# Kernel tuning notes

Measured on AMD Instinct MI355X. Metric: run time of the kernel, lower is better.

## Reference

```python
import jax, jax.numpy as jnp
import numpy as np

D_MODEL = 1024
D_HEAD = 128
BATCH = 4
SEQ = 4096


def setup_inputs() -> dict:
    key = jax.random.key(0)
    ks = jax.random.split(key, 7)
    s = 1.0 / np.sqrt(D_MODEL)
    return {
        "x": jax.random.normal(ks[0], (BATCH, SEQ, D_MODEL), dtype=jnp.float32),
        "Wq": jax.random.normal(ks[1], (D_MODEL, D_HEAD), dtype=jnp.float32) * s,
        "bq": jax.random.normal(ks[2], (D_HEAD,), dtype=jnp.float32) * 0.02,
        "Wk": jax.random.normal(ks[3], (D_MODEL, D_HEAD), dtype=jnp.float32) * s,
        "bk": jax.random.normal(ks[4], (D_HEAD,), dtype=jnp.float32) * 0.02,
        "Wv": jax.random.normal(ks[5], (D_MODEL, D_HEAD), dtype=jnp.float32) * s,
        "bv": jax.random.normal(ks[6], (D_HEAD,), dtype=jnp.float32) * 0.02,
    }


def reference(x, Wq, bq, Wk, bk, Wv, bv):
    # Single-head causal self-attention (intended math of MaskedAttention).
    # x: [B, S, D_MODEL]; projections to [B, S, D_HEAD].
    q = x @ Wq + bq
    k = x @ Wk + bk
    v = x @ Wv + bv
    scale = 1.0 / jnp.sqrt(jnp.asarray(D_HEAD, dtype=x.dtype))
    scores = jnp.einsum("bsd,btd->bst", q, k) * scale  # [B, S, S]
    # additive causal mask: -inf strictly above the diagonal
    s_len = scores.shape[-1]
    causal = jnp.tril(jnp.ones((s_len, s_len), dtype=bool))
    scores = jnp.where(causal[None, :, :], scores, jnp.asarray(-jnp.inf, dtype=scores.dtype))
    attn = jax.nn.softmax(scores, axis=-1)
    return jnp.einsum("bst,btd->bsd", attn, v)  # [B, S, D_HEAD]
```

## Files before the change

kernel.cpp:

```cpp
#include <hip/hip_runtime.h>
#include <stdint.h>
#include <stddef.h>

#define SEQ 4096
#define DM 1024
#define DH 128
#define NB 4
#define SPLITS 4

typedef __attribute__((ext_vector_type(8))) short bf16x8;
typedef __attribute__((ext_vector_type(4))) float f32x4;

__device__ __forceinline__ unsigned short f2bf(float f) {
    union { float f; uint32_t u; } v; v.f = f;
    uint32_t u = v.u + 0x7FFF + ((v.u >> 16) & 1);
    return (unsigned short)(u >> 16);
}

__device__ __forceinline__ void gload_lds16(const void* g, void* l) {
    __builtin_amdgcn_global_load_lds(
        (const __attribute__((address_space(1))) void*)g,
        (__attribute__((address_space(3))) void*)l, 16, 0, 0);
}

__global__ __launch_bounds__(256) void prep_kernel(
    const float* __restrict__ x,
    const float* __restrict__ Wq, const float* __restrict__ Wk,
    const float* __restrict__ Wv,
    unsigned short* __restrict__ xb, unsigned short* __restrict__ Wt)
{
    int bid = blockIdx.x, tid = threadIdx.x;
    if (bid < 1536) {
        int idx = bid * 256 + tid;
        int n = idx >> 10, k = idx & 1023;
        int p = n >> 7, c = n & 127;
        const float* W = (p == 0) ? Wq : (p == 1) ? Wk : Wv;
        Wt[idx] = f2bf(W[k * DH + c]);
    } else {
        size_t i = (size_t)(bid - 1536) * 256 + tid;
        const float* src = x + i * 8;
        bf16x8 o;
        #pragma unroll
        for (int j = 0; j < 8; ++j) o[j] = (short)f2bf(src[j]);
        *(bf16x8*)(xb + i * 8) = o;
    }
}

__global__ __launch_bounds__(256) void proj_kernel(
    const unsigned short* __restrict__ xb,
    const unsigned short* __restrict__ Wt,
    const float* __restrict__ bq, const float* __restrict__ bk,
    const float* __restrict__ bv,
    unsigned short* __restrict__ qb, unsigned short* __restrict__ kb,
    unsigned short* __restrict__ vt)
{
    __shared__ unsigned short A_lds[128 * 64];
    __shared__ unsigned short B_lds[128 * 64];
    const int tid = threadIdx.x;
    const int lane = tid & 63, w = tid >> 6;
    const int wr = w >> 1, wc = w & 1;
    const int q15 = lane & 15, g = lane >> 4;
    const int mt = blockIdx.x & 127, nt = blockIdx.x >> 7;

    f32x4 acc[4][4];
    #pragma unroll
    for (int i = 0; i < 4; ++i)
        #pragma unroll
        for (int j2 = 0; j2 < 4; ++j2) acc[i][j2] = (f32x4){0.f, 0.f, 0.f, 0.f};

    const int arow = tid >> 3, aseg = tid & 7;
    for (int kt = 0; kt < 16; ++kt) {
        #pragma unroll
        for (int i = 0; i < 4; ++i) {
            gload_lds16(xb + ((size_t)(mt * 128 + arow + i * 32) * DM + kt * 64 + aseg * 8),
                        (char*)A_lds + w * 1024 + i * 4096);
            gload_lds16(Wt + ((size_t)(nt * 128 + arow + i * 32) * DM + kt * 64 + aseg * 8),
                        (char*)B_lds + w * 1024 + i * 4096);
        }
        __syncthreads();
        #pragma unroll
        for (int kk = 0; kk < 2; ++kk) {
            bf16x8 af[4], bfr[4];
            #pragma unroll
            for (int mi = 0; mi < 4; ++mi)
                af[mi] = *(const bf16x8*)&A_lds[(wr * 64 + mi * 16 + q15) * 64 + kk * 32 + g * 8];
            #pragma unroll
            for (int ni = 0; ni < 4; ++ni)
                bfr[ni] = *(const bf16x8*)&B_lds[(wc * 64 + ni * 16 + q15) * 64 + kk * 32 + g * 8];
            #pragma unroll
            for (int mi = 0; mi < 4; ++mi)
                #pragma unroll
                for (int ni = 0; ni < 4; ++ni)
                    acc[mi][ni] = __builtin_amdgcn_mfma_f32_16x16x32_bf16(
                        af[mi], bfr[ni], acc[mi][ni], 0, 0, 0);
        }
        __syncthreads();
    }
    const float* bias = (nt == 0) ? bq : (nt == 1) ? bk : bv;
    unsigned short* dst = (nt == 0) ? qb : kb;
    #pragma unroll
    for (int ni = 0; ni < 4; ++ni) {
        int nloc = wc * 64 + ni * 16 + q15;
        float bval = bias[nloc];
        #pragma unroll
        for (int mi = 0; mi < 4; ++mi) {
            int m0 = mt * 128 + wr * 64 + mi * 16 + g * 4;
            #pragma unroll
            for (int r = 0; r < 4; ++r) {
                unsigned short h = f2bf(acc[mi][ni][r] + bval);
                int m = m0 + r;
                if (nt < 2) dst[(size_t)m * DH + nloc] = h;
                else {
                    int b = m >> 12, s = m & 4095;
                    vt[(size_t)(b * 128 + nloc) * SEQ + s] = h;
                }
            }
        }
    }
}

__global__ __launch_bounds__(256) void attn_kernel(
    const unsigned short* __restrict__ qb,
    const unsigned short* __restrict__ kb,
    const unsigned short* __restrict__ vt,
    float* __restrict__ po,
    float* __restrict__ pm, float* __restrict__ pl)
{
    __shared__ unsigned short K_lds[64 * 136];
    __shared__ unsigned short V_lds[128 * 72];
    __shared__ unsigned short P_lds[4 * 16 * 72];
    const int tid = threadIdx.x;
    const int lane = tid & 63, w = tid >> 6;
    const int q15 = lane & 15, g = lane >> 4;
    const int b = blockIdx.x >> 8;
    const int u = blockIdx.x & 255;
    const int j = 63 - (u >> 2);
    const int s = u & 3;
    const int n = j + 1;
    const int lo = (n * s) >> 2, hi = (n * (s + 1)) >> 2;
    if (lo >= hi) return;
    const int qbase = j * 64;

    bf16x8 qf[4];
    const unsigned short* qrow = qb + (size_t)(b * SEQ + qbase + w * 16 + q15) * DH;
    #pragma unroll
    for (int kk = 0; kk < 4; ++kk) qf[kk] = *(const bf16x8*)(qrow + kk * 32 + g * 8);

    f32x4 o[8];
    #pragma unroll
    for (int f = 0; f < 8; ++f) o[f] = (f32x4){0.f, 0.f, 0.f, 0.f};
    float m_run = -__builtin_inff(), l_run = 0.f;
    const float scale = 0.08838834764831845f;
    const int qglob = qbase + w * 16 + q15;

    const int krow = tid >> 4, kseg = tid & 15;
    const int vrow = tid >> 3, vseg = tid & 7;
    const unsigned short* kbb = kb + (size_t)b * SEQ * DH;
    const unsigned short* vbb = vt + (size_t)b * 128 * SEQ;
    bf16x8 kreg[4], vreg[4];
    {
        const unsigned short* ksrc = kbb + (size_t)(lo * 64) * DH;
        const unsigned short* vsrc = vbb + lo * 64;
        #pragma unroll
        for (int i = 0; i < 4; ++i) {
            kreg[i] = *(const bf16x8*)(ksrc + (size_t)(krow + i * 16) * DH + kseg * 8);
            vreg[i] = *(const bf16x8*)(vsrc + (size_t)(vrow + i * 32) * SEQ + vseg * 8);
        }
    }

    for (int kt = lo; kt < hi; ++kt) {
        #pragma unroll
        for (int i = 0; i < 4; ++i) {
            *(bf16x8*)&K_lds[(krow + i * 16) * 136 + kseg * 8] = kreg[i];
            *(bf16x8*)&V_lds[(vrow + i * 32) * 72 + vseg * 8] = vreg[i];
        }
        __syncthreads();
        if (kt + 1 < hi) {
            const unsigned short* ksrc = kbb + (size_t)((kt + 1) * 64) * DH;
            const unsigned short* vsrc = vbb + (kt + 1) * 64;
            #pragma unroll
            for (int i = 0; i < 4; ++i) {
                kreg[i] = *(const bf16x8*)(ksrc + (size_t)(krow + i * 16) * DH + kseg * 8);
                vreg[i] = *(const bf16x8*)(vsrc + (size_t)(vrow + i * 32) * SEQ + vseg * 8);
            }
        }
        f32x4 sf[4];
        #pragma unroll
        for (int mt2 = 0; mt2 < 4; ++mt2) {
            f32x4 sa = (f32x4){0.f, 0.f, 0.f, 0.f};
            #pragma unroll
            for (int kk = 0; kk < 4; ++kk) {
                bf16x8 kf = *(const bf16x8*)&K_lds[(mt2 * 16 + q15) * 136 + kk * 32 + g * 8];
                sa = __builtin_amdgcn_mfma_f32_16x16x32_bf16(kf, qf[kk], sa, 0, 0, 0);
            }
            sf[mt2] = sa;
        }
        float tmax = -__builtin_inff();
        #pragma unroll
        for (int mt2 = 0; mt2 < 4; ++mt2)
            #pragma unroll
            for (int r = 0; r < 4; ++r) {
                int kglob = kt * 64 + mt2 * 16 + g * 4 + r;
                float v = sf[mt2][r] * scale;
                v = (kglob <= qglob) ? v : -__builtin_inff();
                sf[mt2][r] = v;
                tmax = fmaxf(tmax, v);
            }
        tmax = fmaxf(tmax, __shfl_xor(tmax, 16));
        tmax = fmaxf(tmax, __shfl_xor(tmax, 32));
        if (!__all((tmax - m_run) <= 8.0f)) {
            float m_new = fmaxf(m_run, tmax);
            float c = __expf(m_run - m_new);
            float cr[4];
            #pragma unroll
            for (int r = 0; r < 4; ++r) cr[r] = __shfl(c, g * 4 + r);
            #pragma unroll
            for (int f = 0; f < 8; ++f)
                #pragma unroll
                for (int r = 0; r < 4; ++r) o[f][r] *= cr[r];
            l_run *= c;
            m_run = m_new;
        }
        float rsum = 0.f;
        #pragma unroll
        for (int mt2 = 0; mt2 < 4; ++mt2)
            #pragma unroll
            for (int r = 0; r < 4; ++r) {
                float p = __expf(sf[mt2][r] - m_run);
                sf[mt2][r] = p;
                rsum += p;
            }
        rsum += __shfl_xor(rsum, 16);
        rsum += __shfl_xor(rsum, 32);
        l_run += rsum;
        uint32_t* pbase = (uint32_t*)&P_lds[(w * 16 + q15) * 72];
        #pragma unroll
        for (int mt2 = 0; mt2 < 4; ++mt2) {
            uint32_t p01 = (uint32_t)f2bf(sf[mt2][0]) | ((uint32_t)f2bf(sf[mt2][1]) << 16);
            uint32_t p23 = (uint32_t)f2bf(sf[mt2][2]) | ((uint32_t)f2bf(sf[mt2][3]) << 16);
            int e = mt2 * 16 + g * 4;
            pbase[e >> 1] = p01;
            pbase[(e >> 1) + 1] = p23;
        }
        bf16x8 pf[2];
        #pragma unroll
        for (int kk2 = 0; kk2 < 2; ++kk2)
            pf[kk2] = *(const bf16x8*)&P_lds[(w * 16 + q15) * 72 + kk2 * 32 + g * 8];
        #pragma unroll
        for (int f = 0; f < 8; ++f)
            #pragma unroll
            for (int kk2 = 0; kk2 < 2; ++kk2) {
                bf16x8 vf = *(const bf16x8*)&V_lds[(f * 16 + q15) * 72 + kk2 * 32 + g * 8];
                o[f] = __builtin_amdgcn_mfma_f32_16x16x32_bf16(pf[kk2], vf, o[f], 0, 0, 0);
            }
        __syncthreads();
    }
    float* pob = po + ((size_t)(s * NB + b) * SEQ + qbase + w * 16) * DH;
    #pragma unroll
    for (int f = 0; f < 8; ++f)
        #pragma unroll
        for (int r = 0; r < 4; ++r)
            pob[(size_t)(g * 4 + r) * DH + f * 16 + q15] = o[f][r];
    if (g == 0) {
        size_t sidx = (size_t)(s * NB + b) * SEQ + qbase + w * 16 + q15;
        pm[sidx] = m_run;
        pl[sidx] = l_run;
    }
}

__global__ __launch_bounds__(256) void reduce_kernel(
    const float* __restrict__ po, const float* __restrict__ pm,
    const float* __restrict__ pl, float* __restrict__ out)
{
    int r = blockIdx.x * 8 + (threadIdx.x >> 5);
    int d0 = (threadIdx.x & 31) * 4;
    int b = r >> 12, q = r & 4095;
    int n = (q >> 6) + 1;
    float ms[SPLITS];
    float M = -__builtin_inff();
    #pragma unroll
    for (int s = 0; s < SPLITS; ++s) {
        int lo = (n * s) >> 2, hi = (n * (s + 1)) >> 2;
        if (hi > lo) {
            ms[s] = pm[(size_t)(s * NB + b) * SEQ + q];
            M = fmaxf(M, ms[s]);
        } else ms[s] = -__builtin_inff();
    }
    float L = 0.f;
    f32x4 acc = (f32x4){0.f, 0.f, 0.f, 0.f};
    #pragma unroll
    for (int s = 0; s < SPLITS; ++s) {
        int lo = (n * s) >> 2, hi = (n * (s + 1)) >> 2;
        if (hi > lo) {
            float wgt = __expf(ms[s] - M);
            L += wgt * pl[(size_t)(s * NB + b) * SEQ + q];
            f32x4 p = *(const f32x4*)&po[((size_t)(s * NB + b) * SEQ + q) * DH + d0];
            acc += wgt * p;
        }
    }
    float inv = 1.0f / L;
    *(f32x4*)&out[((size_t)(b * SEQ) + q) * DH + d0] = acc * inv;
}

extern "C" void kernel_launch(void* const* d_in, const int* in_sizes, int n_in,
                              void* d_out, int out_size, void* d_ws, size_t ws_size,
                              hipStream_t stream)
{
    const float* x  = (const float*)d_in[0];
    const float* Wq = (const float*)d_in[1];
    const float* bq = (const float*)d_in[2];
    const float* Wk = (const float*)d_in[3];
    const float* bk = (const float*)d_in[4];
    const float* Wv = (const float*)d_in[5];
    const float* bv = (const float*)d_in[6];

    char* ws = (char*)d_ws;
    unsigned short* xb = (unsigned short*)(ws);
    unsigned short* Wt = (unsigned short*)(ws + 33554432);
    unsigned short* qb = (unsigned short*)(ws + 34340864);
    unsigned short* kb = (unsigned short*)(ws + 38535168);
    unsigned short* vt = (unsigned short*)(ws + 42729472);
    float* po = (float*)(ws);
    float* pm = (float*)(ws + 33554432);
    float* pl = (float*)(ws + 33554432 + 262144);

    prep_kernel<<<9728, 256, 0, stream>>>(x, Wq, Wk, Wv, xb, Wt);
    proj_kernel<<<384, 256, 0, stream>>>(xb, Wt, bq, bk, bv, qb, kb, vt);
    attn_kernel<<<1024, 256, 0, stream>>>(qb, kb, vt, po, pm, pl);
    reduce_kernel<<<2048, 256, 0, stream>>>(po, pm, pl, (float*)d_out);
}
```

Before: 198.9 us.

## Read K/V fragments directly from global, fold scale into Wq, remap blocks to XCDs

Drops the shared-memory staging of K and V tiles, and with it the block-wide barriers. Each wave now loads its MFMA fragments straight from global memory and relies on L2/cache reuse across the four waves. The softmax scale is folded into Wq and bq during prep and projection, and the causal mask is applied only on the diagonal tile. Block indices are remapped so each XCD handles one batch's K/V, which improves L2 locality, at the risk of redundant global traffic and exposed load latency now that there is no prefetch.

```diff
diff --git a/kernel.cpp b/kernel.cpp
--- a/kernel.cpp
+++ b/kernel.cpp
@@ -35,7 +35,9 @@
         int n = idx >> 10, k = idx & 1023;
         int p = n >> 7, c = n & 127;
         const float* W = (p == 0) ? Wq : (p == 1) ? Wk : Wv;
-        Wt[idx] = f2bf(W[k * DH + c]);
+        float v = W[k * DH + c];
+        if (p == 0) v *= 0.08838834764831845f;
+        Wt[idx] = f2bf(v);
     } else {
         size_t i = (size_t)(bid - 1536) * 256 + tid;
         const float* src = x + i * 8;
@@ -98,10 +100,11 @@
     }
     const float* bias = (nt == 0) ? bq : (nt == 1) ? bk : bv;
     unsigned short* dst = (nt == 0) ? qb : kb;
+    const float bscale = (nt == 0) ? 0.08838834764831845f : 1.0f;
     #pragma unroll
     for (int ni = 0; ni < 4; ++ni) {
         int nloc = wc * 64 + ni * 16 + q15;
-        float bval = bias[nloc];
+        float bval = bias[nloc] * bscale;
         #pragma unroll
         for (int mi = 0; mi < 4; ++mi) {
             int m0 = mt * 128 + wr * 64 + mi * 16 + g * 4;
@@ -126,20 +129,20 @@
     float* __restrict__ po,
     float* __restrict__ pm, float* __restrict__ pl)
 {
-    __shared__ unsigned short K_lds[64 * 136];
-    __shared__ unsigned short V_lds[128 * 72];
     __shared__ unsigned short P_lds[4 * 16 * 72];
     const int tid = threadIdx.x;
-    const int lane = tid & 63, w = tid >> 6;
+    const int w = tid >> 6;
+    const int lane = tid & 63;
     const int q15 = lane & 15, g = lane >> 4;
-    const int b = blockIdx.x >> 8;
-    const int u = blockIdx.x & 255;
-    const int j = 63 - (u >> 2);
-    const int s = u & 3;
+    const int xcd = blockIdx.x & 7, slot = blockIdx.x >> 3;
+    const int b = xcd >> 1;
+    const int j = 63 - (slot >> 1);
+    const int s = (slot & 1) * 2 + (xcd & 1);
     const int n = j + 1;
     const int lo = (n * s) >> 2, hi = (n * (s + 1)) >> 2;
     if (lo >= hi) return;
     const int qbase = j * 64;
+    const int qglob = qbase + w * 16 + q15;
 
     bf16x8 qf[4];
     const unsigned short* qrow = qb + (size_t)(b * SEQ + qbase + w * 16 + q15) * DH;
@@ -150,62 +153,41 @@
     #pragma unroll
     for (int f = 0; f < 8; ++f) o[f] = (f32x4){0.f, 0.f, 0.f, 0.f};
     float m_run = -__builtin_inff(), l_run = 0.f;
-    const float scale = 0.08838834764831845f;
-    const int qglob = qbase + w * 16 + q15;
-
-    const int krow = tid >> 4, kseg = tid & 15;
-    const int vrow = tid >> 3, vseg = tid & 7;
-    const unsigned short* kbb = kb + (size_t)b * SEQ * DH;
-    const unsigned short* vbb = vt + (size_t)b * 128 * SEQ;
-    bf16x8 kreg[4], vreg[4];
-    {
-        const unsigned short* ksrc = kbb + (size_t)(lo * 64) * DH;
-        const unsigned short* vsrc = vbb + lo * 64;
-        #pragma unroll
-        for (int i = 0; i < 4; ++i) {
-            kreg[i] = *(const bf16x8*)(ksrc + (size_t)(krow + i * 16) * DH + kseg * 8);
-            vreg[i] = *(const bf16x8*)(vsrc + (size_t)(vrow + i * 32) * SEQ + vseg * 8);
-        }
-    }
+
+    const unsigned short* Kb = kb + (size_t)b * SEQ * DH;
+    const unsigned short* Vb = vt + (size_t)b * 128 * SEQ;
+    unsigned short* Pw = &P_lds[w * 16 * 72];
 
     for (int kt = lo; kt < hi; ++kt) {
-        #pragma unroll
-        for (int i = 0; i < 4; ++i) {
-            *(bf16x8*)&K_lds[(krow + i * 16) * 136 + kseg * 8] = kreg[i];
-            *(bf16x8*)&V_lds[(vrow + i * 32) * 72 + vseg * 8] = vreg[i];
-        }
-        __syncthreads();
-        if (kt + 1 < hi) {
-            const unsigned short* ksrc = kbb + (size_t)((kt + 1) * 64) * DH;
-            const unsigned short* vsrc = vbb + (kt + 1) * 64;
-            #pragma unroll
-            for (int i = 0; i < 4; ++i) {
-                kreg[i] = *(const bf16x8*)(ksrc + (size_t)(krow + i * 16) * DH + kseg * 8);
-                vreg[i] = *(const bf16x8*)(vsrc + (size_t)(vrow + i * 32) * SEQ + vseg * 8);
-            }
-        }
+        const unsigned short* Kt = Kb + (size_t)kt * 64 * DH;
         f32x4 sf[4];
         #pragma unroll
         for (int mt2 = 0; mt2 < 4; ++mt2) {
             f32x4 sa = (f32x4){0.f, 0.f, 0.f, 0.f};
             #pragma unroll
             for (int kk = 0; kk < 4; ++kk) {
-                bf16x8 kf = *(const bf16x8*)&K_lds[(mt2 * 16 + q15) * 136 + kk * 32 + g * 8];
+                bf16x8 kf = *(const bf16x8*)(Kt + (size_t)(mt2 * 16 + q15) * DH + kk * 32 + g * 8);
                 sa = __builtin_amdgcn_mfma_f32_16x16x32_bf16(kf, qf[kk], sa, 0, 0, 0);
             }
             sf[mt2] = sa;
         }
         float tmax = -__builtin_inff();
-        #pragma unroll
-        for (int mt2 = 0; mt2 < 4; ++mt2)
-            #pragma unroll
-            for (int r = 0; r < 4; ++r) {
-                int kglob = kt * 64 + mt2 * 16 + g * 4 + r;
-                float v = sf[mt2][r] * scale;
-                v = (kglob <= qglob) ? v : -__builtin_inff();
-                sf[mt2][r] = v;
-                tmax = fmaxf(tmax, v);
-            }
+        if (kt == j) {
+            #pragma unroll
+            for (int mt2 = 0; mt2 < 4; ++mt2)
+                #pragma unroll
+                for (int r = 0; r < 4; ++r) {
+                    int kglob = kt * 64 + mt2 * 16 + g * 4 + r;
+                    float v = (kglob <= qglob) ? sf[mt2][r] : -__builtin_inff();
+                    sf[mt2][r] = v;
+                    tmax = fmaxf(tmax, v);
+                }
+        } else {
+            #pragma unroll
+            for (int mt2 = 0; mt2 < 4; ++mt2)
+                #pragma unroll
+                for (int r = 0; r < 4; ++r) tmax = fmaxf(tmax, sf[mt2][r]);
+        }
         tmax = fmaxf(tmax, __shfl_xor(tmax, 16));
         tmax = fmaxf(tmax, __shfl_xor(tmax, 32));
         if (!__all((tmax - m_run) <= 8.0f)) {
@@ -233,7 +215,7 @@
         rsum += __shfl_xor(rsum, 16);
         rsum += __shfl_xor(rsum, 32);
         l_run += rsum;
-        uint32_t* pbase = (uint32_t*)&P_lds[(w * 16 + q15) * 72];
+        uint32_t* pbase = (uint32_t*)&Pw[q15 * 72];
         #pragma unroll
         for (int mt2 = 0; mt2 < 4; ++mt2) {
             uint32_t p01 = (uint32_t)f2bf(sf[mt2][0]) | ((uint32_t)f2bf(sf[mt2][1]) << 16);
@@ -242,18 +224,19 @@
             pbase[e >> 1] = p01;
             pbase[(e >> 1) + 1] = p23;
         }
+        asm volatile("s_waitcnt lgkmcnt(0)" ::: "memory");
         bf16x8 pf[2];
         #pragma unroll
         for (int kk2 = 0; kk2 < 2; ++kk2)
-            pf[kk2] = *(const bf16x8*)&P_lds[(w * 16 + q15) * 72 + kk2 * 32 + g * 8];
-        #pragma unroll
-        for (int f = 0; f < 8; ++f)
+            pf[kk2] = *(const bf16x8*)&Pw[q15 * 72 + kk2 * 32 + g * 8];
+        #pragma unroll
+        for (int f = 0; f < 8; ++f) {
             #pragma unroll
             for (int kk2 = 0; kk2 < 2; ++kk2) {
-                bf16x8 vf = *(const bf16x8*)&V_lds[(f * 16 + q15) * 72 + kk2 * 32 + g * 8];
+                bf16x8 vf = *(const bf16x8*)(Vb + (size_t)(f * 16 + q15) * SEQ + kt * 64 + kk2 * 32 + g * 8);
                 o[f] = __builtin_amdgcn_mfma_f32_16x16x32_bf16(pf[kk2], vf, o[f], 0, 0, 0);
             }
-        __syncthreads();
+        }
     }
     float* pob = po + ((size_t)(s * NB + b) * SEQ + qbase + w * 16) * DH;
     #pragma unroll
```

Measured after the change: 301.1 us. 1.51x slower.
